# Kernel optimization log

Hardware: AMD Instinct MI355X
Metric: run time of the kernel (lower is better)

## Reference

```python
import jax, jax.numpy as jnp
import numpy as np

T, D_MODEL, NH, DH, NE, TOPK, DHID = 8192, 1024, 8, 128, 8, 2, 512

def setup_inputs() -> dict:
    key = jax.random.key(0)
    ks = jax.random.split(key, 6)
    s = 0.02
    return {
        'x': jax.random.normal(ks[0], (T, D_MODEL), jnp.float32),
        'in_w': jax.random.normal(ks[1], (NH * DH, D_MODEL), jnp.float32) * s,
        'in_b': jnp.zeros((NH * DH,), jnp.float32),
        'router_w': jax.random.normal(ks[2], (NH, NE, DH), jnp.float32) * s,
        'w_in': jax.random.normal(ks[3], (NH, NE, DHID, DH), jnp.float32) * s,
        'w_out': jax.random.normal(ks[4], (NH, NE, DHID, DH), jnp.float32) * s,
        'out_w': jax.random.normal(ks[5], (D_MODEL, NH * DH), jnp.float32) * s,
        'out_b': jnp.zeros((D_MODEL,), jnp.float32),
    }

def reference(x, in_w, in_b, router_w, w_in, w_out, out_w, out_b):
    # Project to latent heads: (T, Nh, dh)
    h = (x @ in_w.T + in_b).reshape(T, NH, DH)
    # Router logits in fp32 (router_fp32=True, no bias, no jitter)
    logits = jnp.einsum('tnd,ned->tne', h.astype(jnp.float32), router_w.astype(jnp.float32))
    vals, idx = jax.lax.top_k(logits, TOPK)            # (T, Nh, k)
    w = jax.nn.softmax(vals, axis=-1).astype(h.dtype)   # (T, Nh, k)
    # Combine top-k weights into a dense per-expert gate (T, Nh, Ne)
    gate = jnp.sum(jax.nn.one_hot(idx, NE, dtype=h.dtype) * w[..., None], axis=2)
    # Expert FFN: y = gelu(x W_in^T) W_out  (exact erf gelu as torch F.gelu)
    hid = jax.nn.gelu(jnp.einsum('tnd,nefd->tnef', h, w_in), approximate=False)  # (T,Nh,Ne,DHID)
    ye = jnp.einsum('tnef,nefd->tned', hid, w_out)       # (T, Nh, Ne, dh)
    y = jnp.einsum('tne,tned->tnd', gate, ye)            # weighted scatter-combine
    # Output projection back to d_model
    return y.reshape(T, NH * DH) @ out_w.T + out_b
```

## Files before the change

kernel.cpp:

```cpp
#include <hip/hip_runtime.h>
#include <hip/hip_bf16.h>
#include <cmath>

#define T_TOK 8192
#define DMODEL 1024
#define NHEAD 8
#define DH 128
#define NEXP 8
#define NNE 64
#define DHID 512

typedef __bf16 bf16x8 __attribute__((ext_vector_type(8)));
typedef float f32x4 __attribute__((ext_vector_type(4)));
typedef unsigned short u16x8 __attribute__((ext_vector_type(8)));

#define GLDS16(g, l) __builtin_amdgcn_global_load_lds( \
    (const __attribute__((address_space(1))) unsigned int*)(g), \
    (__attribute__((address_space(3))) unsigned int*)(l), 16, 0, 0)

static __device__ inline unsigned short f2bf(float f) {
  return __builtin_bit_cast(unsigned short, __float2bfloat16(f));
}
static __device__ inline float bf2f(unsigned short u) {
  unsigned int v = ((unsigned int)u) << 16;
  return __builtin_bit_cast(float, v);
}

static __device__ inline float gelu_f(float v) {
  const float u = v * 0.70710678118654752f;
  const float s = fabsf(u);
  const float t = __builtin_amdgcn_rcpf(fmaf(0.3275911f, s, 1.0f));
  const float e = __expf(-s * s);
  float p = fmaf(1.061405429f, t, -1.453152027f);
  p = fmaf(p, t, 1.421413741f);
  p = fmaf(p, t, -0.284496736f);
  p = fmaf(p, t, 0.254829592f);
  p = p * t;
  const float erfs = fmaf(-p, e, 1.0f);
  const float erfv = copysignf(erfs, u);
  return 0.5f * v * (1.0f + erfv);
}

__global__ __launch_bounds__(256) void prep_kernel(
    const float* __restrict__ x, const float* __restrict__ in_w,
    const float* __restrict__ out_w, const float* __restrict__ w_in,
    const float* __restrict__ wout_src, const float* __restrict__ in_b,
    const float* __restrict__ router_w,
    unsigned short* __restrict__ x_bf, unsigned short* __restrict__ inw_bf,
    unsigned short* __restrict__ outw_bf, unsigned short* __restrict__ win_bf,
    unsigned short* __restrict__ woutT, double* __restrict__ Rtp, double* __restrict__ lb)
{
  __shared__ __align__(16) char smem[17408];
  const int bid = blockIdx.x;
  const int tid = threadIdx.x;

  if (bid < NNE) {
    float (*ws)[DH+4] = (float(*)[DH+4])smem;
    const int ne = bid;
    const float* src = wout_src + (size_t)ne*DHID*DH;
    unsigned short* dst = woutT + (size_t)ne*DH*DHID;
    for (int fc = 0; fc < DHID; fc += 32) {
      __syncthreads();
      for (int i = tid; i < 32*DH; i += 256) {
        const int f = i >> 7, d = i & 127;
        ws[f][d] = src[(size_t)(fc+f)*DH + d];
      }
      __syncthreads();
      for (int i = tid; i < 32*DH; i += 256) {
        const int d = i >> 5, f = i & 31;
        dst[(size_t)d*DHID + fc + f] = f2bf(ws[f][d]);
      }
    }
  } else if (bid < NNE + 32) {
    double (*rw)[DH] = (double(*)[DH])smem;
    const int rbid = bid - NNE;
    const int n  = rbid >> 2;
    const int w  = tid >> 6;
    const int lane = tid & 63;
    const int js = ((rbid & 3) << 2) + w;
    const int j = js*64 + lane;
    for (int i = tid; i < 8*DH; i += 256)
      rw[i >> 7][i & 127] = (double)router_w[(size_t)(n*8 + (i >> 7))*DH + (i & 127)];
    __syncthreads();
    double acc[8];
    #pragma unroll
    for (int e = 0; e < 8; ++e) acc[e] = 0.0;
    const float* wp = in_w + (size_t)(n*DH)*DMODEL + j;
    #pragma unroll 8
    for (int d = 0; d < DH; ++d) {
      const double wv = (double)wp[(size_t)d*DMODEL];
      #pragma unroll
      for (int e = 0; e < 8; ++e) acc[e] += wv * rw[e][d];
    }
    #pragma unroll
    for (int e = 0; e < 8; ++e)
      Rtp[(size_t)(j >> 1)*128 + (n*8 + e)*2 + (j & 1)] = acc[e];
    if (js == 0 && lane < 8) {
      double a = 0.0;
      for (int d = 0; d < DH; ++d) a += (double)in_b[n*DH + d] * rw[lane][d];
      lb[n*8 + lane] = a;
    }
  } else {
    const int N0 = T_TOK*DMODEL/8;
    const int N1 = N0 + DMODEL*DMODEL/8;
    const int N2 = N1 + DMODEL*DMODEL/8;
    const int N3 = N2 + NNE*DHID*DH/8;
    const int nblk = 992 - 96;
    for (int i = (bid - 96)*256 + tid; i < N3; i += nblk*256) {
      const float* s; unsigned short* d; int o;
      if (i < N0)      { s = x;     d = x_bf;    o = i; }
      else if (i < N1) { s = in_w;  d = inw_bf;  o = i - N0; }
      else if (i < N2) { s = out_w; d = outw_bf; o = i - N1; }
      else             { s = w_in;  d = win_bf;  o = i - N2; }
      const float4 a = *((const float4*)s + (size_t)o*2);
      const float4 b = *((const float4*)s + (size_t)o*2 + 1);
      u16x8 v;
      v[0]=f2bf(a.x); v[1]=f2bf(a.y); v[2]=f2bf(a.z); v[3]=f2bf(a.w);
      v[4]=f2bf(b.x); v[5]=f2bf(b.y); v[6]=f2bf(b.z); v[7]=f2bf(b.w);
      *((u16x8*)d + o) = v;
    }
  }
}

__global__ __launch_bounds__(64) void router_partial(
    const float* __restrict__ x, const double* __restrict__ Rtp,
    double* __restrict__ part)
{
  const int bid = blockIdx.x;
  const int s  = bid & 3;
  const int tg = bid >> 2;
  const int t0 = tg << 3;
  const int k0 = s << 8;
  const int lane = threadIdx.x;

  double acc[8];
  #pragma unroll
  for (int t = 0; t < 8; ++t) acc[t] = 0.0;

  const float*  xb = x + (size_t)t0*DMODEL + k0;
  const double* rb = Rtp + (size_t)(k0 >> 1)*128 + lane*2;

  #pragma unroll 2
  for (int kc = 0; kc < 256; kc += 8) {
    const double* r = rb + (size_t)(kc >> 1)*128;
    const double2 r0 = *(const double2*)(r);
    const double2 r1 = *(const double2*)(r + 128);
    const double2 r2 = *(const double2*)(r + 256);
    const double2 r3 = *(const double2*)(r + 384);
    #pragma unroll
    for (int t = 0; t < 8; ++t) {
      const float4 xa = *(const float4*)(xb + (size_t)t*DMODEL + kc);
      const float4 xc = *(const float4*)(xb + (size_t)t*DMODEL + kc + 4);
      acc[t] += (double)xa.x * r0.x;
      acc[t] += (double)xa.y * r0.y;
      acc[t] += (double)xa.z * r1.x;
      acc[t] += (double)xa.w * r1.y;
      acc[t] += (double)xc.x * r2.x;
      acc[t] += (double)xc.y * r2.y;
      acc[t] += (double)xc.z * r3.x;
      acc[t] += (double)xc.w * r3.y;
    }
  }
  #pragma unroll
  for (int t = 0; t < 8; ++t)
    part[((size_t)s*T_TOK + t0 + t)*NNE + lane] = acc[t];
}

__global__ __launch_bounds__(256) void router_top2(
    const double* __restrict__ part, const double* __restrict__ lb,
    int* __restrict__ counts, int* __restrict__ lists, float* __restrict__ wbuf)
{
  __shared__ int lcnt[NNE];
  __shared__ int lbase[NNE];
  const int tid = threadIdx.x;
  const int u = blockIdx.x*256 + tid;
  const int tok = u >> 3;
  const int head = u & 7;
  if (tid < NNE) lcnt[tid] = 0;
  __syncthreads();

  const size_t base = (size_t)tok*NNE + head*8;
  double l[NEXP];
  #pragma unroll
  for (int e = 0; e < NEXP; e += 2) {
    double2 p0 = *(const double2*)(part + base + e);
    double2 p1 = *(const double2*)(part + (size_t)T_TOK*NNE   + base + e);
    double2 p2 = *(const double2*)(part + (size_t)2*T_TOK*NNE + base + e);
    double2 p3 = *(const double2*)(part + (size_t)3*T_TOK*NNE + base + e);
    l[e]   = (((p0.x + p1.x) + p2.x) + p3.x) + lb[head*8 + e];
    l[e+1] = (((p0.y + p1.y) + p2.y) + p3.y) + lb[head*8 + e + 1];
  }
  int e1 = 0; double v1 = l[0];
  #pragma unroll
  for (int e = 1; e < NEXP; ++e) if (l[e] > v1) { v1 = l[e]; e1 = e; }
  int e2 = -1; double v2 = -1.0e300;
  #pragma unroll
  for (int e = 0; e < NEXP; ++e) if (e != e1 && l[e] > v2) { v2 = l[e]; e2 = e; }
  const double ed = exp(v2 - v1);
  const float w1 = (float)(1.0 / (1.0 + ed));
  const float w2 = (float)(ed / (1.0 + ed));
  const int b1 = head*NEXP + e1, b2 = head*NEXP + e2;

  wbuf[(size_t)(tok*NHEAD + head)*2 + 0] = w1;
  wbuf[(size_t)(tok*NHEAD + head)*2 + 1] = w2;

  const int p1i = atomicAdd(&lcnt[b1], 1);
  const int p2i = atomicAdd(&lcnt[b2], 1);
  __syncthreads();
  if (tid < NNE) lbase[tid] = atomicAdd(&counts[tid], lcnt[tid]);
  __syncthreads();
  lists[(size_t)b1*T_TOK + lbase[b1] + p1i] = tok*2;
  lists[(size_t)b2*T_TOK + lbase[b2] + p2i] = tok*2 + 1;
}

__global__ __launch_bounds__(256) void gemm_bf16(
    const unsigned short* __restrict__ A, const unsigned short* __restrict__ B,
    const float* __restrict__ bias, unsigned short* __restrict__ C,
    const int M, const int N, const int K)
{
  __shared__ __align__(16) unsigned short As[128*32];
  __shared__ __align__(16) unsigned short Bs[128*32];
  const int t = threadIdx.x;
  const int lane = t & 63, w = t >> 6;
  const int bm = blockIdx.y << 7, bn = blockIdx.x << 7;
  const int wm = (w & 1) << 6, wn = (w >> 1) << 6;
  f32x4 acc[4][4];
  #pragma unroll
  for (int i = 0; i < 4; ++i)
    #pragma unroll
    for (int j = 0; j < 4; ++j)
      acc[i][j] = (f32x4){0.f, 0.f, 0.f, 0.f};

  const int srow = t >> 2;
  const int skb = (t & 3) << 3;
  const unsigned short* gA = A + (size_t)(bm + srow)*K + skb;
  const unsigned short* gB = B + (size_t)(bn + srow)*K + skb;
  const size_t rowK64 = (size_t)64*K;
  char* lA = (char*)As + t*16;
  char* lB = (char*)Bs + t*16;
  const int rlo = lane & 15;
  const int khi = (lane >> 4) << 4;

  for (int k0 = 0; k0 < K; k0 += 32) {
    GLDS16(gA + k0,          lA);
    GLDS16(gA + rowK64 + k0, lA + 4096);
    GLDS16(gB + k0,          lB);
    GLDS16(gB + rowK64 + k0, lB + 4096);
    __syncthreads();
    bf16x8 av[4], bv[4];
    #pragma unroll
    for (int i = 0; i < 4; ++i) {
      av[i] = *(const bf16x8*)((const char*)As + (wm + i*16 + rlo)*64 + khi);
      bv[i] = *(const bf16x8*)((const char*)Bs + (wn + i*16 + rlo)*64 + khi);
    }
    #pragma unroll
    for (int i = 0; i < 4; ++i)
      #pragma unroll
      for (int j = 0; j < 4; ++j)
        acc[i][j] = __builtin_amdgcn_mfma_f32_16x16x32_bf16(av[i], bv[j], acc[i][j], 0, 0, 0);
    __syncthreads();
  }
  const int rq = (lane >> 4) << 2;
  #pragma unroll
  for (int j = 0; j < 4; ++j) {
    const int col = bn + wn + j*16 + rlo;
    const float bb = bias[col];
    #pragma unroll
    for (int i = 0; i < 4; ++i) {
      const int row0 = bm + wm + i*16 + rq;
      #pragma unroll
      for (int r = 0; r < 4; ++r)
        C[(size_t)(row0 + r)*N + col] = f2bf(acc[i][j][r] + bb);
    }
  }
}

__global__ __launch_bounds__(256) void gemm_out(
    const unsigned short* __restrict__ ye, const unsigned short* __restrict__ B,
    const float* __restrict__ bias, float* __restrict__ C)
{
  const int N = DMODEL, K = DMODEL;
  __shared__ __align__(16) unsigned short As[128*32];
  __shared__ __align__(16) unsigned short Bs[128*32];
  const int t = threadIdx.x;
  const int lane = t & 63, w = t >> 6;
  const int bm = blockIdx.y << 7, bn = blockIdx.x << 7;
  const int wm = (w & 1) << 6, wn = (w >> 1) << 6;
  f32x4 acc[4][4];
  #pragma unroll
  for (int i = 0; i < 4; ++i)
    #pragma unroll
    for (int j = 0; j < 4; ++j)
      acc[i][j] = (f32x4){0.f, 0.f, 0.f, 0.f};

  const int srow = t >> 2;
  const int skb = (t & 3) << 3;
  const unsigned short* gB = B + (size_t)(bn + srow)*K + skb;
  const size_t rowK64 = (size_t)64*K;
  char* lB = (char*)Bs + t*16;
  const int arow = t >> 1;
  const int akh  = (t & 1) << 4;
  const int rlo = lane & 15;
  const int khi = (lane >> 4) << 4;

  for (int k0 = 0; k0 < K; k0 += 32) {
    GLDS16(gB + k0,          lB);
    GLDS16(gB + rowK64 + k0, lB + 4096);
    {
      const int kk = k0 + akh;
      const size_t rbase = (((size_t)(bm + arow)*NHEAD + (kk >> 7))*2)*DH + (kk & 127);
      const u16x8 a0 = *(const u16x8*)(ye + rbase);
      const u16x8 a1 = *(const u16x8*)(ye + rbase + 8);
      const u16x8 b0 = *(const u16x8*)(ye + rbase + DH);
      const u16x8 b1 = *(const u16x8*)(ye + rbase + DH + 8);
      u16x8 s0, s1;
      #pragma unroll
      for (int j = 0; j < 8; ++j) {
        s0[j] = f2bf(bf2f(a0[j]) + bf2f(b0[j]));
        s1[j] = f2bf(bf2f(a1[j]) + bf2f(b1[j]));
      }
      *(u16x8*)((char*)As + arow*64 + akh*2)      = s0;
      *(u16x8*)((char*)As + arow*64 + akh*2 + 16) = s1;
    }
    __syncthreads();
    bf16x8 av[4], bv[4];
    #pragma unroll
    for (int i = 0; i < 4; ++i) {
      av[i] = *(const bf16x8*)((const char*)As + (wm + i*16 + rlo)*64 + khi);
      bv[i] = *(const bf16x8*)((const char*)Bs + (wn + i*16 + rlo)*64 + khi);
    }
    #pragma unroll
    for (int i = 0; i < 4; ++i)
      #pragma unroll
      for (int j = 0; j < 4; ++j)
        acc[i][j] = __builtin_amdgcn_mfma_f32_16x16x32_bf16(av[i], bv[j], acc[i][j], 0, 0, 0);
    __syncthreads();
  }
  const int rq = (lane >> 4) << 2;
  #pragma unroll
  for (int j = 0; j < 4; ++j) {
    const int col = bn + wn + j*16 + rlo;
    const float bb = bias[col];
    #pragma unroll
    for (int i = 0; i < 4; ++i) {
      const int row0 = bm + wm + i*16 + rq;
      #pragma unroll
      for (int r = 0; r < 4; ++r)
        C[(size_t)(row0 + r)*N + col] = acc[i][j][r] + bb;
    }
  }
}

__global__ __launch_bounds__(512, 4) void ffn_mfma_kernel(
    const unsigned short* __restrict__ h_bf, const unsigned short* __restrict__ win_bf,
    const unsigned short* __restrict__ woutT_bf, const int* __restrict__ counts,
    const int* __restrict__ lists, const float* __restrict__ wbuf,
    unsigned short* __restrict__ ye_buf)
{
  const int ne = blockIdx.x;
  const int n  = ne >> 3;
  const int cnt = counts[ne];
  const int t0 = blockIdx.y << 7;
  if (t0 >= cnt) return;
  const int nt = min(128, cnt - t0);

  __shared__ __align__(16) unsigned short hA[128*128];
  __shared__ __align__(16) unsigned short wInS[64*128];
  __shared__ __align__(16) unsigned short wOutS[128*64];
  __shared__ __align__(16) unsigned short hidS[128*64];

  const int t = threadIdx.x;
  const int lane = t & 63, w = t >> 6;
  const long lbase = (long)ne * T_TOK;

  #pragma unroll
  for (int s = 0; s < 4; ++s) {
    const int o = s*8192 + t*16;
    const int row = o >> 8;
    const int c = (t & 15) ^ (row & 7);
    const int trow = t0 + row;
    const int ts = lists[lbase + (trow < cnt ? trow : t0)];
    const unsigned short* g = h_bf + (size_t)(ts >> 1)*DMODEL + n*DH + c*8;
    GLDS16(g, (char*)hA + o);
  }

  const unsigned short* winB  = win_bf  + (size_t)ne*DHID*DH;
  const unsigned short* woutB = woutT_bf + (size_t)ne*DH*DHID;

  const int wm = (w & 3) << 5;
  const int wf = (w >> 2) << 5;
  const int wd = (w >> 2) << 6;
  const int rlo = lane & 15;
  const int kq  = lane >> 4;

  int aAddr[2][4];
  #pragma unroll
  for (int i = 0; i < 2; ++i) {
    const int tr = wm + i*16 + rlo;
    #pragma unroll
    for (int ks = 0; ks < 4; ++ks)
      aAddr[i][ks] = tr*256 + ((ks*64 + kq*16) ^ ((tr & 7) << 4));
  }
  int bAddr[2][4];
  #pragma unroll
  for (int j = 0; j < 2; ++j) {
    const int fr = wf + j*16 + rlo;
    #pragma unroll
    for (int ks = 0; ks < 4; ++ks)
      bAddr[j][ks] = fr*256 + ((ks*64 + kq*16) ^ ((fr & 7) << 4));
  }
  int hWAddr[2][2];
  #pragma unroll
  for (int j = 0; j < 2; ++j)
    #pragma unroll
    for (int i = 0; i < 2; ++i) {
      const int tcol = wm + i*16 + rlo;
      const int fb   = wf + j*16 + kq*4;
      hWAddr[j][i] = tcol*128 + ((fb*2) ^ ((tcol & 7) << 4));
    }
  int a2Addr[2][2];
  #pragma unroll
  for (int i = 0; i < 2; ++i) {
    const int tr = wm + i*16 + rlo;
    #pragma unroll
    for (int ks = 0; ks < 2; ++ks)
      a2Addr[i][ks] = tr*128 + ((ks*64 + kq*16) ^ ((tr & 7) << 4));
  }
  int b2Addr[4][2];
  #pragma unroll
  for (int j = 0; j < 4; ++j) {
    const int dr = wd + j*16 + rlo;
    #pragma unroll
    for (int ks = 0; ks < 2; ++ks)
      b2Addr[j][ks] = dr*128 + ((ks*64 + kq*16) ^ ((dr & 7) << 4));
  }

  auto stage_win = [&](int fc) {
    #pragma unroll
    for (int s = 0; s < 2; ++s) {
      const int o = s*8192 + t*16;
      const int row = o >> 8;
      const int c = (t & 15) ^ (row & 7);
      GLDS16(winB + (size_t)(fc + row)*DH + c*8, (char*)wInS + o);
    }
  };
  auto stage_wout = [&](int fc) {
    #pragma unroll
    for (int s = 0; s < 2; ++s) {
      const int o = s*8192 + t*16;
      const int row = o >> 7;
      const int c = (t & 7) ^ (row & 7);
      GLDS16(woutB + (size_t)row*DHID + fc + c*8, (char*)wOutS + o);
    }
  };

  f32x4 acc2[4][2];
  #pragma unroll
  for (int j = 0; j < 4; ++j)
    #pragma unroll
    for (int i = 0; i < 2; ++i)
      acc2[j][i] = (f32x4){0.f, 0.f, 0.f, 0.f};

  stage_win(0);
  stage_wout(0);
  __syncthreads();

  bf16x8 aReg[2][2];
  #pragma unroll
  for (int i = 0; i < 2; ++i)
    #pragma unroll
    for (int ks = 0; ks < 2; ++ks)
      aReg[i][ks] = *(const bf16x8*)((const char*)hA + aAddr[i][ks]);

  for (int fc = 0; fc < DHID; fc += 64) {
    f32x4 acc1[2][2];
    #pragma unroll
    for (int j = 0; j < 2; ++j)
      #pragma unroll
      for (int i = 0; i < 2; ++i)
        acc1[j][i] = (f32x4){0.f,0.f,0.f,0.f};
    #pragma unroll
    for (int ks = 0; ks < 4; ++ks) {
      bf16x8 a[2], b[2];
      #pragma unroll
      for (int i = 0; i < 2; ++i)
        a[i] = (ks < 2) ? aReg[i][ks]
             : *(const bf16x8*)((const char*)hA + aAddr[i][ks]);
      #pragma unroll
      for (int j = 0; j < 2; ++j)
        b[j] = *(const bf16x8*)((const char*)wInS + bAddr[j][ks]);
      #pragma unroll
      for (int j = 0; j < 2; ++j)
        #pragma unroll
        for (int i = 0; i < 2; ++i)
          acc1[j][i] = __builtin_amdgcn_mfma_f32_16x16x32_bf16(b[j], a[i], acc1[j][i], 0, 0, 0);
    }
    #pragma unroll
    for (int j = 0; j < 2; ++j)
      #pragma unroll
      for (int i = 0; i < 2; ++i) {
        const float g0 = gelu_f(acc1[j][i][0]);
        const float g1 = gelu_f(acc1[j][i][1]);
        const float g2 = gelu_f(acc1[j][i][2]);
        const float g3 = gelu_f(acc1[j][i][3]);
        const unsigned int lo = (unsigned int)f2bf(g0) | ((unsigned int)f2bf(g1) << 16);
        const unsigned int hi = (unsigned int)f2bf(g2) | ((unsigned int)f2bf(g3) << 16);
        *(uint2*)((char*)hidS + hWAddr[j][i]) = make_uint2(lo, hi);
      }
    __syncthreads();

    if (fc + 64 < DHID) stage_win(fc + 64);

    #pragma unroll
    for (int ks = 0; ks < 2; ++ks) {
      bf16x8 a[2], b[4];
      #pragma unroll
      for (int i = 0; i < 2; ++i)
        a[i] = *(const bf16x8*)((const char*)hidS + a2Addr[i][ks]);
      #pragma unroll
      for (int j = 0; j < 4; ++j)
        b[j] = *(const bf16x8*)((const char*)wOutS + b2Addr[j][ks]);
      #pragma unroll
      for (int j = 0; j < 4; ++j)
        #pragma unroll
        for (int i = 0; i < 2; ++i)
          acc2[j][i] = __builtin_amdgcn_mfma_f32_16x16x32_bf16(b[j], a[i], acc2[j][i], 0, 0, 0);
    }
    __syncthreads();

    if (fc + 64 < DHID) {
      stage_wout(fc + 64);
      __syncthreads();
    }
  }

  #pragma unroll
  for (int i = 0; i < 2; ++i) {
    const int tr = wm + i*16 + rlo;
    if (tr < nt) {
      const int ts = lists[lbase + t0 + tr];
      const float gw = wbuf[(size_t)(ts >> 1)*NHEAD*2 + n*2 + (ts & 1)];
      unsigned short* dst = ye_buf +
          ((((size_t)(ts >> 1))*NHEAD + n)*2 + (ts & 1))*DH + wd + kq*4;
      #pragma unroll
      for (int j = 0; j < 4; ++j) {
        const unsigned int lo = (unsigned int)f2bf(gw*acc2[j][i][0]) |
                                ((unsigned int)f2bf(gw*acc2[j][i][1]) << 16);
        const unsigned int hi = (unsigned int)f2bf(gw*acc2[j][i][2]) |
                                ((unsigned int)f2bf(gw*acc2[j][i][3]) << 16);
        *(uint2*)(dst + j*16) = make_uint2(lo, hi);
      }
    }
  }
}

extern "C" void kernel_launch(void* const* d_in, const int* in_sizes, int n_in,
                              void* d_out, int out_size, void* d_ws, size_t ws_size,
                              hipStream_t stream) {
  const float* x        = (const float*)d_in[0];
  const float* in_w     = (const float*)d_in[1];
  const float* in_b     = (const float*)d_in[2];
  const float* router_w = (const float*)d_in[3];
  const float* w_in     = (const float*)d_in[4];
  const float* w_out    = (const float*)d_in[5];
  const float* out_w    = (const float*)d_in[6];
  const float* out_b    = (const float*)d_in[7];
  float* out = (float*)d_out;

  size_t off = 0;
  char* base = (char*)d_ws;
  auto alloc = [&](size_t bytes) -> void* {
    void* p = base + off;
    off += (bytes + 255) & ~(size_t)255;
    return p;
  };
  unsigned short* h_bf    = (unsigned short*)alloc((size_t)T_TOK*DMODEL*2);
  unsigned short* x_bf    = (unsigned short*)alloc((size_t)T_TOK*DMODEL*2);
  unsigned short* inw_bf  = (unsigned short*)alloc((size_t)DMODEL*DMODEL*2);
  unsigned short* outw_bf = (unsigned short*)alloc((size_t)DMODEL*DMODEL*2);
  unsigned short* win_bf  = (unsigned short*)alloc((size_t)NNE*DHID*DH*2);
  unsigned short* woutT_bf= (unsigned short*)alloc((size_t)NNE*DH*DHID*2);
  unsigned short* ye_buf  = (unsigned short*)alloc((size_t)T_TOK*NHEAD*2*DH*2);
  float*  wbuf   = (float*) alloc((size_t)T_TOK*NHEAD*2*4);
  double* Rtp    = (double*)alloc((size_t)DMODEL*NNE*8);
  double* lb     = (double*)alloc(NNE*8);
  int*    counts = (int*)   alloc(NNE*4);
  int*    lists  = (int*)   alloc((size_t)NNE*T_TOK*4);
  double* part   = (double*)ye_buf;

  hipMemsetAsync(counts, 0, NNE*4, stream);

  prep_kernel<<<992, 256, 0, stream>>>(x, in_w, out_w, w_in, w_out, in_b, router_w,
                                       x_bf, inw_bf, outw_bf, win_bf,
                                       woutT_bf, Rtp, lb);

  router_partial<<<4096, 64, 0, stream>>>(x, Rtp, part);
  router_top2<<<T_TOK*NHEAD/256, 256, 0, stream>>>(part, lb, counts, lists, wbuf);

  gemm_bf16<<<dim3(DMODEL/128, T_TOK/128), 256, 0, stream>>>(
      x_bf, inw_bf, in_b, h_bf, T_TOK, DMODEL, DMODEL);

  ffn_mfma_kernel<<<dim3(NNE, T_TOK/128), 512, 0, stream>>>(
      h_bf, win_bf, woutT_bf, counts, lists, wbuf, ye_buf);

  gemm_out<<<dim3(DMODEL/128, T_TOK/128), 256, 0, stream>>>(
      ye_buf, outw_bf, out_b, out);
}
```

Baseline: 256.5 us.

## Reduce router split-K partials in LDS and deepen in-proj GEMM K-tile with swizzle

The router logit kernel now runs four K-slices as waves of one block and sums them in shared memory, writing final logits with the bias added. This removes the 4x partial-sum buffer write and re-read that router_top2 used to do. Separately, the input-projection bf16 GEMM moves from a 32-wide to a 64-wide K tile, with XOR-swizzled LDS placement to avoid bank conflicts. That halves the number of barriers per K and doubles LDS use per block. The summation order of the router partials is unchanged, so top-2 selection should match.

```diff
diff --git a/kernel.cpp b/kernel.cpp
--- a/kernel.cpp
+++ b/kernel.cpp
@@ -122,16 +122,16 @@
   }
 }
 
-__global__ __launch_bounds__(64) void router_partial(
+__global__ __launch_bounds__(256) void router_logits(
     const float* __restrict__ x, const double* __restrict__ Rtp,
-    double* __restrict__ part)
+    const double* __restrict__ lb, double* __restrict__ logits)
 {
-  const int bid = blockIdx.x;
-  const int s  = bid & 3;
-  const int tg = bid >> 2;
-  const int t0 = tg << 3;
-  const int k0 = s << 8;
-  const int lane = threadIdx.x;
+  __shared__ double red[4][8][66];
+  const int tid = threadIdx.x;
+  const int wv = tid >> 6;
+  const int lane = tid & 63;
+  const int t0 = blockIdx.x << 3;
+  const int k0 = wv << 8;
 
   double acc[8];
   #pragma unroll
@@ -162,12 +162,20 @@
     }
   }
   #pragma unroll
-  for (int t = 0; t < 8; ++t)
-    part[((size_t)s*T_TOK + t0 + t)*NNE + lane] = acc[t];
+  for (int t = 0; t < 8; ++t) red[wv][t][lane] = acc[t];
+  __syncthreads();
+  #pragma unroll
+  for (int p = 0; p < 2; ++p) {
+    const int u = tid + p*256;
+    const int tok = u >> 6, ne = u & 63;
+    const double v = ((red[0][tok][ne] + red[1][tok][ne]) + red[2][tok][ne])
+                     + red[3][tok][ne];
+    logits[(size_t)(t0 + tok)*NNE + ne] = v + lb[ne];
+  }
 }
 
 __global__ __launch_bounds__(256) void router_top2(
-    const double* __restrict__ part, const double* __restrict__ lb,
+    const double* __restrict__ logits,
     int* __restrict__ counts, int* __restrict__ lists, float* __restrict__ wbuf)
 {
   __shared__ int lcnt[NNE];
@@ -179,16 +187,12 @@
   if (tid < NNE) lcnt[tid] = 0;
   __syncthreads();
 
-  const size_t base = (size_t)tok*NNE + head*8;
+  const double* l8 = logits + (size_t)tok*NNE + head*8;
   double l[NEXP];
   #pragma unroll
   for (int e = 0; e < NEXP; e += 2) {
-    double2 p0 = *(const double2*)(part + base + e);
-    double2 p1 = *(const double2*)(part + (size_t)T_TOK*NNE   + base + e);
-    double2 p2 = *(const double2*)(part + (size_t)2*T_TOK*NNE + base + e);
-    double2 p3 = *(const double2*)(part + (size_t)3*T_TOK*NNE + base + e);
-    l[e]   = (((p0.x + p1.x) + p2.x) + p3.x) + lb[head*8 + e];
-    l[e+1] = (((p0.y + p1.y) + p2.y) + p3.y) + lb[head*8 + e + 1];
+    const double2 p = *(const double2*)(l8 + e);
+    l[e] = p.x; l[e+1] = p.y;
   }
   int e1 = 0; double v1 = l[0];
   #pragma unroll
@@ -218,8 +222,8 @@
     const float* __restrict__ bias, unsigned short* __restrict__ C,
     const int M, const int N, const int K)
 {
-  __shared__ __align__(16) unsigned short As[128*32];
-  __shared__ __align__(16) unsigned short Bs[128*32];
+  __shared__ __align__(16) unsigned short As[128*64];
+  __shared__ __align__(16) unsigned short Bs[128*64];
   const int t = threadIdx.x;
   const int lane = t & 63, w = t >> 6;
   const int bm = blockIdx.y << 7, bn = blockIdx.x << 7;
@@ -231,33 +235,52 @@
     for (int j = 0; j < 4; ++j)
       acc[i][j] = (f32x4){0.f, 0.f, 0.f, 0.f};
 
-  const int srow = t >> 2;
-  const int skb = (t & 3) << 3;
-  const unsigned short* gA = A + (size_t)(bm + srow)*K + skb;
-  const unsigned short* gB = B + (size_t)(bn + srow)*K + skb;
-  const size_t rowK64 = (size_t)64*K;
+  const int srow = t >> 3;
+  const int scol = ((t & 7) ^ (srow & 7)) << 3;
+  const unsigned short* gA = A + (size_t)(bm + srow)*K + scol;
+  const unsigned short* gB = B + (size_t)(bn + srow)*K + scol;
+  const size_t row32 = (size_t)32*K;
   char* lA = (char*)As + t*16;
   char* lB = (char*)Bs + t*16;
   const int rlo = lane & 15;
   const int khi = (lane >> 4) << 4;
 
-  for (int k0 = 0; k0 < K; k0 += 32) {
-    GLDS16(gA + k0,          lA);
-    GLDS16(gA + rowK64 + k0, lA + 4096);
-    GLDS16(gB + k0,          lB);
-    GLDS16(gB + rowK64 + k0, lB + 4096);
+  int aRd[4][2], bRd[4][2];
+  #pragma unroll
+  for (int i = 0; i < 4; ++i) {
+    const int ra = wm + i*16 + rlo;
+    const int rb2 = wn + i*16 + rlo;
+    #pragma unroll
+    for (int ks = 0; ks < 2; ++ks) {
+      aRd[i][ks] = ra*128 + ((ks*64 + khi) ^ ((ra & 7) << 4));
+      bRd[i][ks] = rb2*128 + ((ks*64 + khi) ^ ((rb2 & 7) << 4));
+    }
+  }
+
+  for (int k0 = 0; k0 < K; k0 += 64) {
+    GLDS16(gA + k0,            lA);
+    GLDS16(gA + row32 + k0,    lA + 4096);
+    GLDS16(gA + 2*row32 + k0,  lA + 8192);
+    GLDS16(gA + 3*row32 + k0,  lA + 12288);
+    GLDS16(gB + k0,            lB);
+    GLDS16(gB + row32 + k0,    lB + 4096);
+    GLDS16(gB + 2*row32 + k0,  lB + 8192);
+    GLDS16(gB + 3*row32 + k0,  lB + 12288);
     __syncthreads();
-    bf16x8 av[4], bv[4];
-    #pragma unroll
-    for (int i = 0; i < 4; ++i) {
-      av[i] = *(const bf16x8*)((const char*)As + (wm + i*16 + rlo)*64 + khi);
-      bv[i] = *(const bf16x8*)((const char*)Bs + (wn + i*16 + rlo)*64 + khi);
-    }
-    #pragma unroll
-    for (int i = 0; i < 4; ++i)
-      #pragma unroll
-      for (int j = 0; j < 4; ++j)
-        acc[i][j] = __builtin_amdgcn_mfma_f32_16x16x32_bf16(av[i], bv[j], acc[i][j], 0, 0, 0);
+    #pragma unroll
+    for (int ks = 0; ks < 2; ++ks) {
+      bf16x8 av[4], bv[4];
+      #pragma unroll
+      for (int i = 0; i < 4; ++i) {
+        av[i] = *(const bf16x8*)((const char*)As + aRd[i][ks]);
+        bv[i] = *(const bf16x8*)((const char*)Bs + bRd[i][ks]);
+      }
+      #pragma unroll
+      for (int i = 0; i < 4; ++i)
+        #pragma unroll
+        for (int j = 0; j < 4; ++j)
+          acc[i][j] = __builtin_amdgcn_mfma_f32_16x16x32_bf16(av[i], bv[j], acc[i][j], 0, 0, 0);
+    }
     __syncthreads();
   }
   const int rq = (lane >> 4) << 2;
@@ -586,7 +609,7 @@
   double* lb     = (double*)alloc(NNE*8);
   int*    counts = (int*)   alloc(NNE*4);
   int*    lists  = (int*)   alloc((size_t)NNE*T_TOK*4);
-  double* part   = (double*)ye_buf;
+  double* logits = (double*)ye_buf;
 
   hipMemsetAsync(counts, 0, NNE*4, stream);
 
@@ -594,8 +617,8 @@
                                        x_bf, inw_bf, outw_bf, win_bf,
                                        woutT_bf, Rtp, lb);
 
-  router_partial<<<4096, 64, 0, stream>>>(x, Rtp, part);
-  router_top2<<<T_TOK*NHEAD/256, 256, 0, stream>>>(part, lb, counts, lists, wbuf);
+  router_logits<<<T_TOK/8, 256, 0, stream>>>(x, Rtp, lb, logits);
+  router_top2<<<T_TOK*NHEAD/256, 256, 0, stream>>>(logits, counts, lists, wbuf);
 
   gemm_bf16<<<dim3(DMODEL/128, T_TOK/128), 256, 0, stream>>>(
       x_bf, inw_bf, in_b, h_bf, T_TOK, DMODEL, DMODEL);
```

Result: slower. 285.3 us (+11.2%).
